# Performance work log

Measured on AMD Instinct MI355X. Metric: run time of the kernel, lower is better.

The kernel has to match this reference:

```python
import jax, jax.numpy as jnp
import numpy as np

S = 3072        # total tokens (3 images x 1024 patches)
E = 1280        # n_embed
H = 16          # n_heads
HD = E // H     # head_dim = 80
NSEG = 3


def rotate_half(x):
    x1 = x[..., : x.shape[-1] // 2]
    x2 = x[..., x.shape[-1] // 2 :]
    return jnp.concatenate((-x2, x1), axis=-1)


def setup_inputs() -> dict:
    key = jax.random.key(0)
    ks = jax.random.split(key, 6)
    x = jax.random.normal(ks[0], (S, E), dtype=jnp.float32)
    rotary_pos_emb = jax.random.normal(ks[1], (S, HD // 2), dtype=jnp.float32)
    qkv_w = jax.random.normal(ks[2], (3 * E, E), dtype=jnp.float32) * 0.02
    qkv_b = jax.random.normal(ks[3], (3 * E,), dtype=jnp.float32) * 0.02
    proj_w = jax.random.normal(ks[4], (E, E), dtype=jnp.float32) * 0.02
    proj_b = jax.random.normal(ks[5], (E,), dtype=jnp.float32) * 0.02
    cu_seqlens = (jnp.arange(NSEG + 1, dtype=jnp.int32) * (S // NSEG))  # [0,1024,2048,3072]
    return {"x": x, "rotary_pos_emb": rotary_pos_emb, "qkv_w": qkv_w,
            "qkv_b": qkv_b, "proj_w": proj_w, "proj_b": proj_b,
            "cu_seqlens": cu_seqlens}


def reference(x, rotary_pos_emb, qkv_w, qkv_b, proj_w, proj_b, cu_seqlens):
    seq_len = x.shape[0]
    # qkv projection (torch Linear: x @ W.T + b)
    qkv = (x @ qkv_w.T + qkv_b).reshape(seq_len, 3, H, HD)
    q, k, v = qkv[:, 0], qkv[:, 1], qkv[:, 2]          # each [S, H, HD]

    # inline RoPE: cos/sin repeated over the two halves of head_dim
    cos = jnp.cos(rotary_pos_emb)
    sin = jnp.sin(rotary_pos_emb)
    cos = jnp.concatenate([cos, cos], axis=-1)[:, None, :]  # [S, 1, HD]
    sin = jnp.concatenate([sin, sin], axis=-1)[:, None, :]
    q = q * cos + rotate_half(q) * sin
    k = k * cos + rotate_half(k) * sin

    # block-diagonal segment mask from cu_seqlens
    seg = jnp.searchsorted(cu_seqlens, jnp.arange(seq_len), side="right")  # [S]
    mask = seg[:, None] == seg[None, :]                 # [S, S] bool

    scale = jnp.asarray(1.0 / np.sqrt(HD), dtype=q.dtype)
    scores = jnp.einsum("qhd,khd->hqk", q, k) * scale   # [H, S, S]
    scores = jnp.where(mask[None], scores, jnp.finfo(scores.dtype).min)
    attn = jax.nn.softmax(scores, axis=-1)
    out = jnp.einsum("hqk,khd->qhd", attn, v).reshape(seq_len, E)
    return out @ proj_w.T + proj_b
```

## Files before the change

kernel.cpp:

```cpp
#include <hip/hip_runtime.h>
#include <hip/hip_bf16.h>
#include <math.h>

#define SEQ   3072
#define EMB   1280
#define NHEAD 16
#define HDIM  80
#define QKVN  3840
#define NSEGS 3

typedef __attribute__((ext_vector_type(8))) short bf16x8;
typedef __attribute__((ext_vector_type(4))) short bf16x4;
typedef __attribute__((ext_vector_type(4))) float f32x4;

__device__ __forceinline__ short f2bf(float f) {
    __hip_bfloat16 h = __float2bfloat16(f);
    return *reinterpret_cast<short*>(&h);
}
__device__ __forceinline__ float bf2f(short s) {
    unsigned int u = ((unsigned int)(unsigned short)s) << 16;
    union { unsigned int u; float f; } c; c.u = u;
    return c.f;
}

__device__ __forceinline__ void gload_lds16(const void* g, void* l) {
    __builtin_amdgcn_global_load_lds(
        (const __attribute__((address_space(1))) unsigned int*)g,
        (__attribute__((address_space(3))) unsigned int*)l, 16, 0, 0);
}

__global__ __launch_bounds__(256)
void cvt3_kernel(const float* __restrict__ a, short* __restrict__ oa, int na8,
                 const float* __restrict__ b, short* __restrict__ ob, int nb8,
                 const float* __restrict__ c, short* __restrict__ oc, int nc8)
{
    int j = blockIdx.x * 256 + threadIdx.x;
    const float* src; short* dst;
    if (j < na8) { src = a; dst = oa; }
    else if ((j -= na8) < nb8) { src = b; dst = ob; }
    else { j -= nb8; src = c; dst = oc; }
    float4 x = *reinterpret_cast<const float4*>(&src[j*8]);
    float4 y = *reinterpret_cast<const float4*>(&src[j*8+4]);
    bf16x8 o;
    o[0]=f2bf(x.x); o[1]=f2bf(x.y); o[2]=f2bf(x.z); o[3]=f2bf(x.w);
    o[4]=f2bf(y.x); o[5]=f2bf(y.y); o[6]=f2bf(y.z); o[7]=f2bf(y.w);
    *reinterpret_cast<bf16x8*>(&dst[j*8]) = o;
}

__device__ __forceinline__ void store_val(float v, float* p) { *p = v; }
__device__ __forceinline__ void store_val(float v, short* p) { *p = f2bf(v); }

template<typename OT, bool SWZ>
__global__ __launch_bounds__(256)
void gemm_bf16_nt(const short* __restrict__ A, int lda,
                  const short* __restrict__ B,
                  const float* __restrict__ bias, OT* __restrict__ C,
                  int M, int N, int K)
{
    __shared__ short As0[128][32], Bs0[128][32];
    __shared__ short As1[128][32], Bs1[128][32];

    int bx, by;
    if (SWZ) {
        const int flat = blockIdx.x;
        const int xcd  = flat & 7;
        const int i    = flat >> 3;
        by = xcd * 3 + (i % 3);
        bx = i / 3;
    } else {
        bx = blockIdx.x;
        by = blockIdx.y;
    }

    const int tid = threadIdx.x;
    const int w   = tid >> 6;
    const int l   = tid & 63;
    const int l15 = l & 15;
    const int l4  = l >> 4;
    const int wr  = w >> 1;
    const int wc  = w & 1;
    const int row0 = by * 128;
    const int col0 = bx * 128;

    const int srow = l >> 2;
    const int sk   = (l & 3) * 8;
    const int c0 = w, c1 = w + 4;

    f32x4 acc[4][4];
    #pragma unroll
    for (int mi = 0; mi < 4; ++mi)
        #pragma unroll
        for (int ni = 0; ni < 4; ++ni) acc[mi][ni] = (f32x4){0.f,0.f,0.f,0.f};

#define STAGE_NT(AS, BS, KOFF)                                                          \
    do {                                                                                \
        gload_lds16(&A[(size_t)(row0 + c0*16 + srow) * lda + (KOFF) + sk], &AS[c0*16][0]); \
        gload_lds16(&A[(size_t)(row0 + c1*16 + srow) * lda + (KOFF) + sk], &AS[c1*16][0]); \
        gload_lds16(&B[(size_t)(col0 + c0*16 + srow) * K   + (KOFF) + sk], &BS[c0*16][0]); \
        gload_lds16(&B[(size_t)(col0 + c1*16 + srow) * K   + (KOFF) + sk], &BS[c1*16][0]); \
    } while (0)

#define COMPUTE_NT(AS, BS)                                                              \
    do {                                                                                \
        bf16x8 af[4], bfr[4];                                                           \
        _Pragma("unroll")                                                               \
        for (int mi = 0; mi < 4; ++mi)                                                  \
            af[mi] = *reinterpret_cast<const bf16x8*>(&AS[wr*64 + mi*16 + l15][l4*8]);  \
        _Pragma("unroll")                                                               \
        for (int ni = 0; ni < 4; ++ni)                                                  \
            bfr[ni] = *reinterpret_cast<const bf16x8*>(&BS[wc*64 + ni*16 + l15][l4*8]); \
        _Pragma("unroll")                                                               \
        for (int mi = 0; mi < 4; ++mi)                                                  \
            _Pragma("unroll")                                                           \
            for (int ni = 0; ni < 4; ++ni)                                              \
                acc[mi][ni] = __builtin_amdgcn_mfma_f32_16x16x32_bf16(                  \
                    af[mi], bfr[ni], acc[mi][ni], 0, 0, 0);                             \
    } while (0)

    STAGE_NT(As0, Bs0, 0);
    __syncthreads();

    for (int k0 = 0; k0 < K; k0 += 64) {
        if (k0 + 32 < K) STAGE_NT(As1, Bs1, k0 + 32);
        COMPUTE_NT(As0, Bs0);
        __syncthreads();
        if (k0 + 64 < K) STAGE_NT(As0, Bs0, k0 + 64);
        COMPUTE_NT(As1, Bs1);
        __syncthreads();
    }
#undef STAGE_NT
#undef COMPUTE_NT

    #pragma unroll
    for (int ni = 0; ni < 4; ++ni) {
        int col = col0 + wc*64 + ni*16 + l15;
        float bv = bias[col];
        #pragma unroll
        for (int mi = 0; mi < 4; ++mi) {
            #pragma unroll
            for (int r = 0; r < 4; ++r) {
                size_t row = (size_t)(row0 + wr*64 + mi*16 + l4*4 + r);
                store_val(acc[mi][ni][r] + bv, &C[row * (size_t)N + col]);
            }
        }
    }
}

template<typename OT>
__global__ __launch_bounds__(256)
void gemm_bf16_nt64(const short* __restrict__ A, int lda,
                    const short* __restrict__ B,
                    const float* __restrict__ bias, OT* __restrict__ C,
                    int M, int N, int K)
{
    __shared__ short As0[128][32], Bs0[64][32];
    __shared__ short As1[128][32], Bs1[64][32];

    const int tid = threadIdx.x;
    const int w   = tid >> 6;
    const int l   = tid & 63;
    const int l15 = l & 15;
    const int l4  = l >> 4;
    const int wr  = w >> 1;
    const int wc  = w & 1;
    const int row0 = blockIdx.y * 128;
    const int col0 = blockIdx.x * 64;

    const int srow = l >> 2;
    const int sk   = (l & 3) * 8;
    const int c0 = w, c1 = w + 4;

    f32x4 acc[4][2];
    #pragma unroll
    for (int mi = 0; mi < 4; ++mi)
        #pragma unroll
        for (int ni = 0; ni < 2; ++ni) acc[mi][ni] = (f32x4){0.f,0.f,0.f,0.f};

#define STAGE_NT64(AS, BS, KOFF)                                                        \
    do {                                                                                \
        gload_lds16(&A[(size_t)(row0 + c0*16 + srow) * lda + (KOFF) + sk], &AS[c0*16][0]); \
        gload_lds16(&A[(size_t)(row0 + c1*16 + srow) * lda + (KOFF) + sk], &AS[c1*16][0]); \
        gload_lds16(&B[(size_t)(col0 + w*16  + srow) * K   + (KOFF) + sk], &BS[w*16][0]);  \
    } while (0)

#define COMPUTE_NT64(AS, BS)                                                            \
    do {                                                                                \
        bf16x8 af[4], bfr[2];                                                           \
        _Pragma("unroll")                                                               \
        for (int mi = 0; mi < 4; ++mi)                                                  \
            af[mi] = *reinterpret_cast<const bf16x8*>(&AS[wr*64 + mi*16 + l15][l4*8]);  \
        _Pragma("unroll")                                                               \
        for (int ni = 0; ni < 2; ++ni)                                                  \
            bfr[ni] = *reinterpret_cast<const bf16x8*>(&BS[wc*32 + ni*16 + l15][l4*8]); \
        _Pragma("unroll")                                                               \
        for (int mi = 0; mi < 4; ++mi)                                                  \
            _Pragma("unroll")                                                           \
            for (int ni = 0; ni < 2; ++ni)                                              \
                acc[mi][ni] = __builtin_amdgcn_mfma_f32_16x16x32_bf16(                  \
                    af[mi], bfr[ni], acc[mi][ni], 0, 0, 0);                             \
    } while (0)

    STAGE_NT64(As0, Bs0, 0);
    __syncthreads();

    for (int k0 = 0; k0 < K; k0 += 64) {
        if (k0 + 32 < K) STAGE_NT64(As1, Bs1, k0 + 32);
        COMPUTE_NT64(As0, Bs0);
        __syncthreads();
        if (k0 + 64 < K) STAGE_NT64(As0, Bs0, k0 + 64);
        COMPUTE_NT64(As1, Bs1);
        __syncthreads();
    }
#undef STAGE_NT64
#undef COMPUTE_NT64

    #pragma unroll
    for (int ni = 0; ni < 2; ++ni) {
        int col = col0 + wc*32 + ni*16 + l15;
        float bv = bias[col];
        #pragma unroll
        for (int mi = 0; mi < 4; ++mi) {
            #pragma unroll
            for (int r = 0; r < 4; ++r) {
                size_t row = (size_t)(row0 + wr*64 + mi*16 + l4*4 + r);
                store_val(acc[mi][ni][r] + bv, &C[row * (size_t)N + col]);
            }
        }
    }
}

__global__ __launch_bounds__(256)
void rope_bf16_kernel(short* __restrict__ qkv, const float* __restrict__ rpe)
{
    int idx = blockIdx.x * 256 + threadIdx.x;
    int blk = idx % 5;
    int h   = (idx / 5) % NHEAD;
    int s   = (idx / (5*NHEAD)) % SEQ;
    int t   = idx / (5*NHEAD*SEQ);
    int d0  = blk * 8;

    const float* rp = rpe + s*40 + d0;
    short* p = qkv + (size_t)s*QKVN + t*EMB + h*HDIM + d0;
    bf16x8 v0 = *reinterpret_cast<const bf16x8*>(p);
    bf16x8 v1 = *reinterpret_cast<const bf16x8*>(p + 40);
    bf16x8 o0, o1;
    #pragma unroll
    for (int j = 0; j < 8; ++j) {
        float ang = rp[j];
        float sn = sinf(ang), cs = cosf(ang);
        float a = bf2f(v0[j]), b = bf2f(v1[j]);
        o0[j] = f2bf(a*cs - b*sn);
        o1[j] = f2bf(b*cs + a*sn);
    }
    *reinterpret_cast<bf16x8*>(p)      = o0;
    *reinterpret_cast<bf16x8*>(p + 40) = o1;
}

__global__ __launch_bounds__(256, 4)
void attn_mfma(const short* __restrict__ qkv, const int* __restrict__ cu,
               short* __restrict__ aout)
{
    const int flat = blockIdx.x;
    const int xcd  = flat & 7;
    const int rem  = flat >> 3;
    const int qt   = rem & 15;
    const int shhi = rem >> 4;
    const int sh   = xcd + 8*shhi;
    const int h    = sh / 3;
    const int seg  = sh - 3*h;
    const int s0 = cu[seg], s1 = cu[seg+1];

    const int tid = threadIdx.x;
    const int w   = tid >> 6;
    const int l   = tid & 63;
    const int l15 = l & 15;
    const int l4  = l >> 4;

    __shared__ short Kl[64][128];
    __shared__ short Vt[HDIM][64];

    const int q0 = s0 + qt*64 + w*16;

    bf16x8 bzero;
    #pragma unroll
    for (int j = 0; j < 8; ++j) bzero[j] = 0;

    bf16x8 qf[3];
    {
        const short* qp = qkv + (size_t)(q0 + l15) * QKVN + h*HDIM;
        qf[0] = *reinterpret_cast<const bf16x8*>(qp + l4*8);
        qf[1] = *reinterpret_cast<const bf16x8*>(qp + 32 + l4*8);
        qf[2] = (l4 < 2) ? *reinterpret_cast<const bf16x8*>(qp + 64 + l4*8) : bzero;
    }

    float m = -3.4e38f, lsum = 0.f;
    f32x4 O[5];
    #pragma unroll
    for (int dt = 0; dt < 5; ++dt) O[dt] = (f32x4){0.f,0.f,0.f,0.f};

    int kkey[3], ku[3];
    const short* kptr[3];
    short* klds[3];
    #pragma unroll
    for (int i = 0; i < 3; ++i) {
        int task = tid + i*256;
        kkey[i] = task / 12;
        ku[i]   = task - kkey[i]*12;
        kptr[i] = qkv + (size_t)(s0 + kkey[i])*QKVN + EMB + h*HDIM + ku[i]*8;
        klds[i] = &Kl[kkey[i]][(ku[i] ^ (kkey[i] & 7))*8];
    }

    const int vu  = ((l >> 2) & 3) | ((l >> 5) << 2);
    const int vbs = ((l >> 4) & 1) * 4 + (l & 3);
    const int vd0 = w * 20;
    const short* vp1 = qkv + (size_t)(s0 + l) * QKVN + 2*EMB + h*HDIM + vd0;

    bf16x8 kreg[3];
    bf16x8 vA, vB;
    bf16x4 vC;
    #pragma unroll
    for (int i = 0; i < 3; ++i)
        kreg[i] = (ku[i] < 10) ? *reinterpret_cast<const bf16x8*>(kptr[i]) : bzero;
    vA = *reinterpret_cast<const bf16x8*>(vp1);
    vB = *reinterpret_cast<const bf16x8*>(vp1 + 8);
    vC = *reinterpret_cast<const bf16x4*>(vp1 + 16);

    const float scale2 = 0.1612982054f;
    const int nk = s1 - s0;
    const size_t step = (size_t)64 * QKVN;
    short* vt_flat = &Vt[0][0];

    for (int kc = 0; kc < nk; kc += 64) {
        __syncthreads();

        #pragma unroll
        for (int i = 0; i < 3; ++i)
            *reinterpret_cast<bf16x8*>(klds[i]) = kreg[i];
        #pragma unroll
        for (int e = 0; e < 8; ++e) {
            int d = vd0 + e;
            vt_flat[d*64 + ((vu ^ (d & 7)) & 7)*8 + vbs] = vA[e];
        }
        #pragma unroll
        for (int e = 0; e < 8; ++e) {
            int d = vd0 + 8 + e;
            vt_flat[d*64 + ((vu ^ (d & 7)) & 7)*8 + vbs] = vB[e];
        }
        #pragma unroll
        for (int e = 0; e < 4; ++e) {
            int d = vd0 + 16 + e;
            vt_flat[d*64 + ((vu ^ (d & 7)) & 7)*8 + vbs] = vC[e];
        }

        if (kc + 64 < nk) {
            #pragma unroll
            for (int i = 0; i < 3; ++i) {
                kptr[i] += step;
                if (ku[i] < 10) kreg[i] = *reinterpret_cast<const bf16x8*>(kptr[i]);
            }
            vp1 += step;
            vA = *reinterpret_cast<const bf16x8*>(vp1);
            vB = *reinterpret_cast<const bf16x8*>(vp1 + 8);
            vC = *reinterpret_cast<const bf16x4*>(vp1 + 16);
        }
        __syncthreads();

        f32x4 S[4];
        __builtin_amdgcn_s_setprio(1);
        #pragma unroll
        for (int ct = 0; ct < 4; ++ct) {
            f32x4 acc = (f32x4){0.f,0.f,0.f,0.f};
            int key = ct*16 + l15;
            #pragma unroll
            for (int t = 0; t < 3; ++t) {
                int u = (4*t + l4) ^ (key & 7);
                bf16x8 a = *reinterpret_cast<const bf16x8*>(&Kl[key][u*8]);
                acc = __builtin_amdgcn_mfma_f32_16x16x32_bf16(a, qf[t], acc, 0, 0, 0);
            }
            S[ct] = acc;
        }
        __builtin_amdgcn_s_setprio(0);

        float mxr = -3.4e38f;
        #pragma unroll
        for (int ct = 0; ct < 4; ++ct)
            #pragma unroll
            for (int r = 0; r < 4; ++r) mxr = fmaxf(mxr, S[ct][r]);
        float mx = mxr * scale2;
        mx = fmaxf(mx, __shfl_xor(mx, 16));
        mx = fmaxf(mx, __shfl_xor(mx, 32));
        if (!__all(mx - m <= 8.f)) {
            float mn   = fmaxf(m, mx);
            float corr = exp2f(m - mn);
            lsum *= corr;
            #pragma unroll
            for (int dt = 0; dt < 5; ++dt)
                #pragma unroll
                for (int r = 0; r < 4; ++r) O[dt][r] *= corr;
            m = mn;
        }
        float p[4][4];
        float ps = 0.f;
        #pragma unroll
        for (int ct = 0; ct < 4; ++ct)
            #pragma unroll
            for (int r = 0; r < 4; ++r) {
                float e = exp2f(fmaf(S[ct][r], scale2, -m));
                p[ct][r] = e;
                ps += e;
            }
        ps += __shfl_xor(ps, 16);
        ps += __shfl_xor(ps, 32);
        lsum += ps;

        #pragma unroll
        for (int s2 = 0; s2 < 2; ++s2) {
            bf16x8 pb;
            #pragma unroll
            for (int j = 0; j < 8; ++j)
                pb[j] = f2bf(p[2*s2 + (j>>2)][j & 3]);
            __builtin_amdgcn_s_setprio(1);
            #pragma unroll
            for (int dt = 0; dt < 5; ++dt) {
                int d = dt*16 + l15;
                bf16x8 va = *reinterpret_cast<const bf16x8*>(
                    &vt_flat[d*64 + (((4*s2 + l4) ^ (d & 7)) & 7)*8]);
                O[dt] = __builtin_amdgcn_mfma_f32_16x16x32_bf16(va, pb, O[dt], 0, 0, 0);
            }
            __builtin_amdgcn_s_setprio(0);
        }
    }

    float inv = 1.f / lsum;
    short* orow = aout + (size_t)(q0 + l15) * EMB + h*HDIM;
    #pragma unroll
    for (int dt = 0; dt < 5; ++dt) {
        bf16x4 o4;
        #pragma unroll
        for (int r = 0; r < 4; ++r) o4[r] = f2bf(O[dt][r] * inv);
        *reinterpret_cast<bf16x4*>(&orow[dt*16 + 4*l4]) = o4;
    }
}

extern "C" void kernel_launch(void* const* d_in, const int* in_sizes, int n_in,
                              void* d_out, int out_size, void* d_ws, size_t ws_size,
                              hipStream_t stream)
{
    const float* x      = (const float*)d_in[0];
    const float* rpe    = (const float*)d_in[1];
    const float* qkv_w  = (const float*)d_in[2];
    const float* qkv_b  = (const float*)d_in[3];
    const float* proj_w = (const float*)d_in[4];
    const float* proj_b = (const float*)d_in[5];
    const int*   cu     = (const int*)d_in[6];
    float* out = (float*)d_out;

    short* ws       = (short*)d_ws;
    short* qkv_bf   = ws;
    short* x_bf     = qkv_bf  + (size_t)SEQ * QKVN;
    short* qkvw_bf  = x_bf    + (size_t)SEQ * EMB;
    short* projw_bf = qkvw_bf + (size_t)QKVN * EMB;
    short* attn_bf  = projw_bf+ (size_t)EMB * EMB;

    dim3 blk(256);

    const int na8 = SEQ*EMB/8, nb8 = QKVN*EMB/8, nc8 = EMB*EMB/8;
    cvt3_kernel<<<dim3((na8+nb8+nc8)/256), blk, 0, stream>>>(
        x, x_bf, na8, qkv_w, qkvw_bf, nb8, proj_w, projw_bf, nc8);

    gemm_bf16_nt<short, true><<<dim3((QKVN/128)*(SEQ/128)), blk, 0, stream>>>(
        x_bf, EMB, qkvw_bf, qkv_b, qkv_bf, SEQ, QKVN, EMB);

    rope_bf16_kernel<<<dim3(2*SEQ*NHEAD*5/256), blk, 0, stream>>>(qkv_bf, rpe);

    attn_mfma<<<dim3(16*NSEGS*NHEAD), blk, 0, stream>>>(qkv_bf, cu, attn_bf);

    gemm_bf16_nt64<float><<<dim3(EMB/64, SEQ/128), blk, 0, stream>>>(
        attn_bf, EMB, projw_bf, proj_b, out, SEQ, EMB, EMB);
}
```

Measured before the change: 128.9 us.

## Double-buffer K/V tiles in LDS with one barrier per iteration

Replaces the single K and V^T LDS tiles with two ping-pong buffers. Each iteration writes the next chunk's registers into the alternate buffer before computing on the current one, which removes one of the two __syncthreads per key chunk and lets the LDS stores overlap the MFMA work. LDS use roughly doubles to about 52KB per block, which may reduce the number of resident blocks per CU below the 4 requested in the launch bounds.

```diff
diff --git a/kernel.cpp b/kernel.cpp
--- a/kernel.cpp
+++ b/kernel.cpp
@@ -256,6 +256,8 @@
     *reinterpret_cast<bf16x8*>(p + 40) = o1;
 }
 
+#define ABUF 13312
+
 __global__ __launch_bounds__(256, 4)
 void attn_mfma(const short* __restrict__ qkv, const int* __restrict__ cu,
                short* __restrict__ aout)
@@ -276,8 +278,7 @@
     const int l15 = l & 15;
     const int l4  = l >> 4;
 
-    __shared__ short Kl[64][128];
-    __shared__ short Vt[HDIM][64];
+    __shared__ short lds[2 * ABUF];
 
     const int q0 = s0 + qt*64 + w*16;
 
@@ -298,16 +299,15 @@
     #pragma unroll
     for (int dt = 0; dt < 5; ++dt) O[dt] = (f32x4){0.f,0.f,0.f,0.f};
 
-    int kkey[3], ku[3];
+    int ku[3], kofs[3];
     const short* kptr[3];
-    short* klds[3];
     #pragma unroll
     for (int i = 0; i < 3; ++i) {
         int task = tid + i*256;
-        kkey[i] = task / 12;
-        ku[i]   = task - kkey[i]*12;
-        kptr[i] = qkv + (size_t)(s0 + kkey[i])*QKVN + EMB + h*HDIM + ku[i]*8;
-        klds[i] = &Kl[kkey[i]][(ku[i] ^ (kkey[i] & 7))*8];
+        int key  = task / 12;
+        ku[i]    = task - key*12;
+        kptr[i]  = qkv + (size_t)(s0 + key)*QKVN + EMB + h*HDIM + ku[i]*8;
+        kofs[i]  = key*128 + (ku[i] ^ (key & 7))*8;
     }
 
     const int vu  = ((l >> 2) & 3) | ((l >> 5) << 2);
@@ -315,55 +315,75 @@
     const int vd0 = w * 20;
     const short* vp1 = qkv + (size_t)(s0 + l) * QKVN + 2*EMB + h*HDIM + vd0;
 
+    const float scale2 = 0.1612982054f;
+    const int nk = s1 - s0;
+    const size_t step = (size_t)64 * QKVN;
+
     bf16x8 kreg[3];
     bf16x8 vA, vB;
     bf16x4 vC;
-    #pragma unroll
-    for (int i = 0; i < 3; ++i)
-        kreg[i] = (ku[i] < 10) ? *reinterpret_cast<const bf16x8*>(kptr[i]) : bzero;
-    vA = *reinterpret_cast<const bf16x8*>(vp1);
-    vB = *reinterpret_cast<const bf16x8*>(vp1 + 8);
-    vC = *reinterpret_cast<const bf16x4*>(vp1 + 16);
-
-    const float scale2 = 0.1612982054f;
-    const int nk = s1 - s0;
-    const size_t step = (size_t)64 * QKVN;
-    short* vt_flat = &Vt[0][0];
-
+
+#define LOAD_REGS()                                                             \
+    do {                                                                        \
+        _Pragma("unroll")                                                       \
+        for (int i = 0; i < 3; ++i)                                             \
+            if (ku[i] < 10) kreg[i] = *reinterpret_cast<const bf16x8*>(kptr[i]);\
+        vA = *reinterpret_cast<const bf16x8*>(vp1);                             \
+        vB = *reinterpret_cast<const bf16x8*>(vp1 + 8);                         \
+        vC = *reinterpret_cast<const bf16x4*>(vp1 + 16);                        \
+    } while (0)
+
+#define WRITE_LDS(OFF)                                                          \
+    do {                                                                        \
+        short* kb = &lds[(OFF)];                                                \
+        short* vb = &lds[(OFF) + 8192];                                         \
+        _Pragma("unroll")                                                       \
+        for (int i = 0; i < 3; ++i)                                             \
+            *reinterpret_cast<bf16x8*>(&kb[kofs[i]]) = kreg[i];                 \
+        _Pragma("unroll")                                                       \
+        for (int e = 0; e < 8; ++e) {                                           \
+            int d = vd0 + e;                                                    \
+            vb[d*64 + ((vu ^ (d & 7)) & 7)*8 + vbs] = vA[e];                    \
+        }                                                                       \
+        _Pragma("unroll")                                                       \
+        for (int e = 0; e < 8; ++e) {                                           \
+            int d = vd0 + 8 + e;                                                \
+            vb[d*64 + ((vu ^ (d & 7)) & 7)*8 + vbs] = vB[e];                    \
+        }                                                                       \
+        _Pragma("unroll")                                                       \
+        for (int e = 0; e < 4; ++e) {                                           \
+            int d = vd0 + 16 + e;                                               \
+            vb[d*64 + ((vu ^ (d & 7)) & 7)*8 + vbs] = vC[e];                    \
+        }                                                                       \
+    } while (0)
+
+    #pragma unroll
+    for (int i = 0; i < 3; ++i) kreg[i] = bzero;
+
+    LOAD_REGS();
+    WRITE_LDS(0);
+    if (nk > 64) {
+        #pragma unroll
+        for (int i = 0; i < 3; ++i) kptr[i] += step;
+        vp1 += step;
+        LOAD_REGS();
+    }
+    __syncthreads();
+
+    int curoff = 0;
     for (int kc = 0; kc < nk; kc += 64) {
-        __syncthreads();
-
-        #pragma unroll
-        for (int i = 0; i < 3; ++i)
-            *reinterpret_cast<bf16x8*>(klds[i]) = kreg[i];
-        #pragma unroll
-        for (int e = 0; e < 8; ++e) {
-            int d = vd0 + e;
-            vt_flat[d*64 + ((vu ^ (d & 7)) & 7)*8 + vbs] = vA[e];
+        if (kc + 64 < nk) {
+            WRITE_LDS(curoff ^ ABUF);
+            if (kc + 128 < nk) {
+                #pragma unroll
+                for (int i = 0; i < 3; ++i) kptr[i] += step;
+                vp1 += step;
+                LOAD_REGS();
+            }
         }
-        #pragma unroll
-        for (int e = 0; e < 8; ++e) {
-            int d = vd0 + 8 + e;
-            vt_flat[d*64 + ((vu ^ (d & 7)) & 7)*8 + vbs] = vB[e];
-        }
-        #pragma unroll
-        for (int e = 0; e < 4; ++e) {
-            int d = vd0 + 16 + e;
-            vt_flat[d*64 + ((vu ^ (d & 7)) & 7)*8 + vbs] = vC[e];
-        }
-
-        if (kc + 64 < nk) {
-            #pragma unroll
-            for (int i = 0; i < 3; ++i) {
-                kptr[i] += step;
-                if (ku[i] < 10) kreg[i] = *reinterpret_cast<const bf16x8*>(kptr[i]);
-            }
-            vp1 += step;
-            vA = *reinterpret_cast<const bf16x8*>(vp1);
-            vB = *reinterpret_cast<const bf16x8*>(vp1 + 8);
-            vC = *reinterpret_cast<const bf16x4*>(vp1 + 16);
-        }
-        __syncthreads();
+
+        const short* kb = &lds[curoff];
+        const short* vb = &lds[curoff + 8192];
 
         f32x4 S[4];
         __builtin_amdgcn_s_setprio(1);
@@ -374,7 +394,7 @@
             #pragma unroll
             for (int t = 0; t < 3; ++t) {
                 int u = (4*t + l4) ^ (key & 7);
-                bf16x8 a = *reinterpret_cast<const bf16x8*>(&Kl[key][u*8]);
+                bf16x8 a = *reinterpret_cast<const bf16x8*>(&kb[key*128 + u*8]);
                 acc = __builtin_amdgcn_mfma_f32_16x16x32_bf16(a, qf[t], acc, 0, 0, 0);
             }
             S[ct] = acc;
@@ -424,12 +444,17 @@
             for (int dt = 0; dt < 5; ++dt) {
                 int d = dt*16 + l15;
                 bf16x8 va = *reinterpret_cast<const bf16x8*>(
-                    &vt_flat[d*64 + (((4*s2 + l4) ^ (d & 7)) & 7)*8]);
+                    &vb[d*64 + (((4*s2 + l4) ^ (d & 7)) & 7)*8]);
                 O[dt] = __builtin_amdgcn_mfma_f32_16x16x32_bf16(va, pb, O[dt], 0, 0, 0);
             }
             __builtin_amdgcn_s_setprio(0);
         }
-    }
+
+        __syncthreads();
+        curoff ^= ABUF;
+    }
+#undef LOAD_REGS
+#undef WRITE_LDS
 
     float inv = 1.f / lsum;
     short* orow = aout + (size_t)(q0 + l15) * EMB + h*HDIM;
```

Measured after the change: 131.8 us. 1.02x slower.
